# Kernel optimization log

Hardware: AMD Instinct MI355X
Metric: run time of the kernel (lower is better)

Reference implementation:

```python
import jax, jax.numpy as jnp
import numpy as np

R = 16
ALPHA = 32.0
SCALING = ALPHA / max(1, R)

def setup_inputs() -> dict:
    key = jax.random.key(0)
    ks = jax.random.split(key, 7)
    B_, D, M = 16384, 1024, 4096
    return {
        "x": jax.random.normal(ks[0], (B_, D), dtype=jnp.float32),
        "W0": jax.random.normal(ks[1], (M, D), dtype=jnp.float32) * 0.02,
        "b0": jax.random.normal(ks[2], (M,), dtype=jnp.float32) * 0.02,
        "A": jax.random.normal(ks[3], (R, D), dtype=jnp.float32) * 0.001,
        "B": jax.random.normal(ks[4], (M, R), dtype=jnp.float32) * 0.02,
        "W2": jax.random.normal(ks[5], (1, M), dtype=jnp.float32) * 0.02,
        "b2": jax.random.normal(ks[6], (1,), dtype=jnp.float32) * 0.02,
    }

def reference(x, W0, b0, A, B, W2, b2):
    # effective_W = W0 + scaling * (B @ A)  -> [m_hidden, d_in]
    W_eff = W0 + SCALING * (B @ A)
    # F.linear(x, W_eff, b0): x @ W_eff^T + b0 -> [batch, m_hidden]
    h = jax.nn.relu(jnp.einsum('bd,md->bm', x, W_eff) + b0)
    # fc2: [batch, 1] then squeeze(-1)
    out = (jnp.einsum('bm,om->bo', h, W2) + b2).squeeze(-1)
    return out
```

## Files before the change

### kernel.cpp

```cpp
#include <hip/hip_runtime.h>
#include <hip/hip_bf16.h>
#include <stdint.h>

#define BATCH  16384
#define D_IN   1024
#define M_HID  4096
#define R_LORA 16
#define SCALING 2.0f

#define BM 128
#define BN 128
#define BK 64

typedef __bf16 bf16x8 __attribute__((ext_vector_type(8)));
typedef float  f32x4  __attribute__((ext_vector_type(4)));


__device__ __forceinline__ unsigned short f2bf(float f) {
    union { float f; unsigned int u; } c; c.f = f;
    unsigned int u = c.u;
    return (unsigned short)((u + 0x7FFFu + ((u >> 16) & 1u)) >> 16);
}

#define PREP_X_BLOCKS   (BATCH * D_IN / 8 / 256)
#define PREP_W_BLOCKS   (M_HID * D_IN / 4 / 256)
#define PREP_O_BLOCKS   (BATCH / 256)
__global__ __launch_bounds__(256) void k_prep(
    const float* __restrict__ x, const float* __restrict__ W0,
    const float* __restrict__ A, const float* __restrict__ Bl,
    const float* __restrict__ b2,
    unsigned short* __restrict__ xb, unsigned short* __restrict__ wb,
    float* __restrict__ out)
{
    int bid = blockIdx.x;
    if (bid < PREP_X_BLOCKS) {
        int idx = bid * 256 + threadIdx.x;
        const float4* x4 = (const float4*)x;
        float4 a = x4[2 * idx], b = x4[2 * idx + 1];
        uint4 o;
        o.x = (unsigned)f2bf(a.x) | ((unsigned)f2bf(a.y) << 16);
        o.y = (unsigned)f2bf(a.z) | ((unsigned)f2bf(a.w) << 16);
        o.z = (unsigned)f2bf(b.x) | ((unsigned)f2bf(b.y) << 16);
        o.w = (unsigned)f2bf(b.z) | ((unsigned)f2bf(b.w) << 16);
        ((uint4*)xb)[idx] = o;
    } else if (bid < PREP_X_BLOCKS + PREP_W_BLOCKS) {
        int idx = (bid - PREP_X_BLOCKS) * 256 + threadIdx.x;
        int m  = idx >> 8;
        int d4 = idx & 255;
        float4 acc = ((const float4*)W0)[idx];
        const float* brow = Bl + m * R_LORA;
#pragma unroll
        for (int r = 0; r < R_LORA; ++r) {
            float s = SCALING * brow[r];
            float4 a4 = ((const float4*)(A + r * D_IN))[d4];
            acc.x += s * a4.x; acc.y += s * a4.y; acc.z += s * a4.z; acc.w += s * a4.w;
        }
        uint2 o;
        o.x = (unsigned)f2bf(acc.x) | ((unsigned)f2bf(acc.y) << 16);
        o.y = (unsigned)f2bf(acc.z) | ((unsigned)f2bf(acc.w) << 16);
        ((uint2*)wb)[idx] = o;
    } else {
        int i = (bid - PREP_X_BLOCKS - PREP_W_BLOCKS) * 256 + threadIdx.x;
        out[i] = b2[0];
    }
}

template<bool XBF, bool WBF>
__global__ __launch_bounds__(256) void k_gemm_fused(
    const unsigned short* __restrict__ xb, const float* __restrict__ xf,
    const unsigned short* __restrict__ wb,
    const float* __restrict__ W0, const float* __restrict__ A,
    const float* __restrict__ Bl,
    const float* __restrict__ b0, const float* __restrict__ W2,
    float* __restrict__ out)
{
    __shared__ unsigned short As[BM * BK];
    __shared__ unsigned short Bs[BN * BK];

    const int tid  = threadIdx.x;
    const int lane = tid & 63;
    const int wave = tid >> 6;
    const int col0 = blockIdx.x * BN;
    const int row0 = blockIdx.y * BM;
    const int wm = (wave & 1) * 64;
    const int wn = (wave >> 1) * 64;
    const int cl = lane & 15, q = lane >> 4;

    f32x4 acc[4][4] = {};

    for (int k0 = 0; k0 < D_IN; k0 += BK) {
        if (XBF) {
#pragma unroll
            for (int it = 0; it < 4; ++it) {
                int c = it * 256 + tid;
                int r = c >> 3, s = c & 7;
                int k = s ^ (r & 7);
                const unsigned short* g = xb + (row0 + r) * D_IN + k0 + k * 8;
                __builtin_amdgcn_global_load_lds(
                    (__attribute__((address_space(1))) void*)g,
                    (__attribute__((address_space(3))) void*)(&As[c * 8]),
                    16, 0, 0);
            }
        } else {
#pragma unroll
            for (int it = 0; it < 8; ++it) {
                int gidx = it * 256 + tid;
                int r = gidx >> 4, kc = (gidx & 15) * 4;
                float4 v = *(const float4*)(xf + (size_t)(row0 + r) * D_IN + k0 + kc);
                ushort4 o = make_ushort4(f2bf(v.x), f2bf(v.y), f2bf(v.z), f2bf(v.w));
                int k = kc >> 3, half = (gidx & 1) * 4;
                *(ushort4*)(&As[r * BK + (k ^ (r & 7)) * 8 + half]) = o;
            }
        }
        if (WBF) {
#pragma unroll
            for (int it = 0; it < 4; ++it) {
                int c = it * 256 + tid;
                int r = c >> 3, s = c & 7;
                int k = s ^ (r & 7);
                const unsigned short* g = wb + (col0 + r) * D_IN + k0 + k * 8;
                __builtin_amdgcn_global_load_lds(
                    (__attribute__((address_space(1))) void*)g,
                    (__attribute__((address_space(3))) void*)(&Bs[c * 8]),
                    16, 0, 0);
            }
        } else {
#pragma unroll
            for (int it = 0; it < 8; ++it) {
                int gidx = it * 256 + tid;
                int n = gidx >> 4, kc = (gidx & 15) * 4;
                float4 v = *(const float4*)(W0 + (size_t)(col0 + n) * D_IN + k0 + kc);
                const float* brow = Bl + (col0 + n) * R_LORA;
#pragma unroll
                for (int r = 0; r < R_LORA; ++r) {
                    float s = SCALING * brow[r];
                    float4 a4 = *(const float4*)(A + r * D_IN + k0 + kc);
                    v.x += s * a4.x; v.y += s * a4.y; v.z += s * a4.z; v.w += s * a4.w;
                }
                ushort4 o = make_ushort4(f2bf(v.x), f2bf(v.y), f2bf(v.z), f2bf(v.w));
                int k = kc >> 3, half = (gidx & 1) * 4;
                *(ushort4*)(&Bs[n * BK + (k ^ (n & 7)) * 8 + half]) = o;
            }
        }
        __syncthreads();

#pragma unroll
        for (int kk = 0; kk < BK; kk += 32) {
            const int chunk = (kk >> 3) + q;
            const int sA = chunk ^ (cl & 7);
            bf16x8 af[4], bfr[4];
#pragma unroll
            for (int t = 0; t < 4; ++t)
                af[t] = *(const bf16x8*)(&As[(wm + t * 16 + cl) * BK + sA * 8]);
#pragma unroll
            for (int t = 0; t < 4; ++t)
                bfr[t] = *(const bf16x8*)(&Bs[(wn + t * 16 + cl) * BK + sA * 8]);
#pragma unroll
            for (int ti = 0; ti < 4; ++ti)
#pragma unroll
                for (int tj = 0; tj < 4; ++tj)
                    acc[ti][tj] = __builtin_amdgcn_mfma_f32_16x16x32_bf16(
                        af[ti], bfr[tj], acc[ti][tj], 0, 0, 0);
        }
        __syncthreads();
    }

    const int r_base = row0 + wm + q * 4;
    const int c_base = col0 + wn + cl;
#pragma unroll
    for (int ti = 0; ti < 4; ++ti) {
        float p0 = 0.f, p1 = 0.f, p2 = 0.f, p3 = 0.f;
#pragma unroll
        for (int tj = 0; tj < 4; ++tj) {
            int hid = c_base + tj * 16;
            float w2 = W2[hid], bb = b0[hid];
            f32x4 a = acc[ti][tj];
            p0 += fmaxf(a[0] + bb, 0.f) * w2;
            p1 += fmaxf(a[1] + bb, 0.f) * w2;
            p2 += fmaxf(a[2] + bb, 0.f) * w2;
            p3 += fmaxf(a[3] + bb, 0.f) * w2;
        }
#pragma unroll
        for (int m = 1; m <= 8; m <<= 1) {
            p0 += __shfl_xor(p0, m, 64);
            p1 += __shfl_xor(p1, m, 64);
            p2 += __shfl_xor(p2, m, 64);
            p3 += __shfl_xor(p3, m, 64);
        }
        if (cl == 0) {
            int rr = r_base + ti * 16;
            unsafeAtomicAdd(&out[rr + 0], p0);
            unsafeAtomicAdd(&out[rr + 1], p1);
            unsafeAtomicAdd(&out[rr + 2], p2);
            unsafeAtomicAdd(&out[rr + 3], p3);
        }
    }
}

extern "C" void kernel_launch(void* const* d_in, const int* in_sizes, int n_in,
                              void* d_out, int out_size, void* d_ws, size_t ws_size,
                              hipStream_t stream) {
    const float* x  = (const float*)d_in[0];
    const float* W0 = (const float*)d_in[1];
    const float* b0 = (const float*)d_in[2];
    const float* A  = (const float*)d_in[3];
    const float* Bl = (const float*)d_in[4];
    const float* W2 = (const float*)d_in[5];
    const float* b2 = (const float*)d_in[6];
    float* out = (float*)d_out;

    const size_t wb_bytes = (size_t)M_HID * D_IN * 2;
    const size_t xb_bytes = (size_t)BATCH * D_IN * 2;
    const bool have_ws = ws_size >= wb_bytes + xb_bytes;
    unsigned short* wb = (unsigned short*)d_ws;
    unsigned short* xb = (unsigned short*)((char*)d_ws + wb_bytes);

    dim3 grid(M_HID / BN, BATCH / BM);

    if (have_ws) {
        hipLaunchKernelGGL(k_prep, dim3(PREP_X_BLOCKS + PREP_W_BLOCKS + PREP_O_BLOCKS),
                           dim3(256), 0, stream, x, W0, A, Bl, b2, xb, wb, out);
        hipLaunchKernelGGL((k_gemm_fused<true, true>), grid, dim3(256), 0, stream,
                           xb, x, wb, W0, A, Bl, b0, W2, out);
    } else {
        hipLaunchKernelGGL(k_prep, dim3(PREP_O_BLOCKS), dim3(256), 0, stream,
                           x, W0, A, Bl, b2, xb, wb, out);
        hipLaunchKernelGGL((k_gemm_fused<false, false>), grid, dim3(256), 0, stream,
                           xb, x, wb, W0, A, Bl, b0, W2, out);
    }
}
```

Before: 309.5 us.

## Enlarge GEMM tile to 256x128 with 8 waves and 32x32x16 MFMA

Doubles the row tile to 256 and the block to 512 threads (8 waves), and switches the inner product from 16x16x32 to 32x32x16 bf16 MFMA with 2x2 fragments per wave. Each loaded W tile now serves twice as many rows, and the larger MFMA shape cuts LDS fragment reads per flop. The epilogue now reduces over 32 lanes and issues one atomic per row per wave. The cost is more LDS per block (48KB) and fewer resident blocks. The fallback path also gets a separate init kernel.

```diff
diff --git a/kernel.cpp b/kernel.cpp
--- a/kernel.cpp
+++ b/kernel.cpp
@@ -8,12 +8,13 @@
 #define R_LORA 16
 #define SCALING 2.0f
 
-#define BM 128
+#define BM 256
 #define BN 128
 #define BK 64
+#define NTHREADS 512
 
 typedef __bf16 bf16x8 __attribute__((ext_vector_type(8)));
-typedef float  f32x4  __attribute__((ext_vector_type(4)));
+typedef float  f32x16 __attribute__((ext_vector_type(16)));
 
 
 __device__ __forceinline__ unsigned short f2bf(float f) {
@@ -65,8 +66,13 @@
     }
 }
 
-template<bool XBF, bool WBF>
-__global__ __launch_bounds__(256) void k_gemm_fused(
+__global__ __launch_bounds__(256) void k_init_out(float* __restrict__ out,
+                                                  const float* __restrict__ b2) {
+    out[blockIdx.x * 256 + threadIdx.x] = b2[0];
+}
+
+template<bool FAST>
+__global__ __launch_bounds__(NTHREADS) void k_gemm_fused(
     const unsigned short* __restrict__ xb, const float* __restrict__ xf,
     const unsigned short* __restrict__ wb,
     const float* __restrict__ W0, const float* __restrict__ A,
@@ -82,17 +88,18 @@
     const int wave = tid >> 6;
     const int col0 = blockIdx.x * BN;
     const int row0 = blockIdx.y * BM;
-    const int wm = (wave & 1) * 64;
-    const int wn = (wave >> 1) * 64;
-    const int cl = lane & 15, q = lane >> 4;
-
-    f32x4 acc[4][4] = {};
+    const int wm = (wave & 3) * 64;
+    const int wn = (wave >> 2) * 64;
+    const int rl   = lane & 31;
+    const int half = lane >> 5;
+
+    f32x16 acc[2][2] = {};
 
     for (int k0 = 0; k0 < D_IN; k0 += BK) {
-        if (XBF) {
+        if (FAST) {
 #pragma unroll
             for (int it = 0; it < 4; ++it) {
-                int c = it * 256 + tid;
+                int c = it * NTHREADS + tid;
                 int r = c >> 3, s = c & 7;
                 int k = s ^ (r & 7);
                 const unsigned short* g = xb + (row0 + r) * D_IN + k0 + k * 8;
@@ -101,21 +108,9 @@
                     (__attribute__((address_space(3))) void*)(&As[c * 8]),
                     16, 0, 0);
             }
-        } else {
-#pragma unroll
-            for (int it = 0; it < 8; ++it) {
-                int gidx = it * 256 + tid;
-                int r = gidx >> 4, kc = (gidx & 15) * 4;
-                float4 v = *(const float4*)(xf + (size_t)(row0 + r) * D_IN + k0 + kc);
-                ushort4 o = make_ushort4(f2bf(v.x), f2bf(v.y), f2bf(v.z), f2bf(v.w));
-                int k = kc >> 3, half = (gidx & 1) * 4;
-                *(ushort4*)(&As[r * BK + (k ^ (r & 7)) * 8 + half]) = o;
-            }
-        }
-        if (WBF) {
-#pragma unroll
-            for (int it = 0; it < 4; ++it) {
-                int c = it * 256 + tid;
+#pragma unroll
+            for (int it = 0; it < 2; ++it) {
+                int c = it * NTHREADS + tid;
                 int r = c >> 3, s = c & 7;
                 int k = s ^ (r & 7);
                 const unsigned short* g = wb + (col0 + r) * D_IN + k0 + k * 8;
@@ -127,7 +122,16 @@
         } else {
 #pragma unroll
             for (int it = 0; it < 8; ++it) {
-                int gidx = it * 256 + tid;
+                int gidx = it * NTHREADS + tid;
+                int r = gidx >> 4, kc = (gidx & 15) * 4;
+                float4 v = *(const float4*)(xf + (size_t)(row0 + r) * D_IN + k0 + kc);
+                ushort4 o = make_ushort4(f2bf(v.x), f2bf(v.y), f2bf(v.z), f2bf(v.w));
+                int k = kc >> 3, h4 = (gidx & 1) * 4;
+                *(ushort4*)(&As[r * BK + ((k ^ (r & 7)) * 8) + h4]) = o;
+            }
+#pragma unroll
+            for (int it = 0; it < 4; ++it) {
+                int gidx = it * NTHREADS + tid;
                 int n = gidx >> 4, kc = (gidx & 15) * 4;
                 float4 v = *(const float4*)(W0 + (size_t)(col0 + n) * D_IN + k0 + kc);
                 const float* brow = Bl + (col0 + n) * R_LORA;
@@ -138,61 +142,49 @@
                     v.x += s * a4.x; v.y += s * a4.y; v.z += s * a4.z; v.w += s * a4.w;
                 }
                 ushort4 o = make_ushort4(f2bf(v.x), f2bf(v.y), f2bf(v.z), f2bf(v.w));
-                int k = kc >> 3, half = (gidx & 1) * 4;
-                *(ushort4*)(&Bs[n * BK + (k ^ (n & 7)) * 8 + half]) = o;
+                int k = kc >> 3, h4 = (gidx & 1) * 4;
+                *(ushort4*)(&Bs[n * BK + ((k ^ (n & 7)) * 8) + h4]) = o;
             }
         }
         __syncthreads();
 
 #pragma unroll
-        for (int kk = 0; kk < BK; kk += 32) {
-            const int chunk = (kk >> 3) + q;
-            const int sA = chunk ^ (cl & 7);
-            bf16x8 af[4], bfr[4];
-#pragma unroll
-            for (int t = 0; t < 4; ++t)
-                af[t] = *(const bf16x8*)(&As[(wm + t * 16 + cl) * BK + sA * 8]);
-#pragma unroll
-            for (int t = 0; t < 4; ++t)
-                bfr[t] = *(const bf16x8*)(&Bs[(wn + t * 16 + cl) * BK + sA * 8]);
-#pragma unroll
-            for (int ti = 0; ti < 4; ++ti)
-#pragma unroll
-                for (int tj = 0; tj < 4; ++tj)
-                    acc[ti][tj] = __builtin_amdgcn_mfma_f32_16x16x32_bf16(
+        for (int kk = 0; kk < BK; kk += 16) {
+            const int chunk = (kk >> 3) + half;
+            const int slot  = chunk ^ (rl & 7);
+            bf16x8 af[2], bfr[2];
+#pragma unroll
+            for (int t = 0; t < 2; ++t)
+                af[t] = *(const bf16x8*)(&As[(wm + t * 32 + rl) * BK + slot * 8]);
+#pragma unroll
+            for (int t = 0; t < 2; ++t)
+                bfr[t] = *(const bf16x8*)(&Bs[(wn + t * 32 + rl) * BK + slot * 8]);
+#pragma unroll
+            for (int ti = 0; ti < 2; ++ti)
+#pragma unroll
+                for (int tj = 0; tj < 2; ++tj)
+                    acc[ti][tj] = __builtin_amdgcn_mfma_f32_32x32x16_bf16(
                         af[ti], bfr[tj], acc[ti][tj], 0, 0, 0);
         }
         __syncthreads();
     }
 
-    const int r_base = row0 + wm + q * 4;
-    const int c_base = col0 + wn + cl;
-#pragma unroll
-    for (int ti = 0; ti < 4; ++ti) {
-        float p0 = 0.f, p1 = 0.f, p2 = 0.f, p3 = 0.f;
-#pragma unroll
-        for (int tj = 0; tj < 4; ++tj) {
-            int hid = c_base + tj * 16;
-            float w2 = W2[hid], bb = b0[hid];
-            f32x4 a = acc[ti][tj];
-            p0 += fmaxf(a[0] + bb, 0.f) * w2;
-            p1 += fmaxf(a[1] + bb, 0.f) * w2;
-            p2 += fmaxf(a[2] + bb, 0.f) * w2;
-            p3 += fmaxf(a[3] + bb, 0.f) * w2;
-        }
-#pragma unroll
-        for (int m = 1; m <= 8; m <<= 1) {
-            p0 += __shfl_xor(p0, m, 64);
-            p1 += __shfl_xor(p1, m, 64);
-            p2 += __shfl_xor(p2, m, 64);
-            p3 += __shfl_xor(p3, m, 64);
-        }
-        if (cl == 0) {
-            int rr = r_base + ti * 16;
-            unsafeAtomicAdd(&out[rr + 0], p0);
-            unsafeAtomicAdd(&out[rr + 1], p1);
-            unsafeAtomicAdd(&out[rr + 2], p2);
-            unsafeAtomicAdd(&out[rr + 3], p3);
+    const int hid0 = col0 + wn + rl;
+    const float w2a = W2[hid0],      bba = b0[hid0];
+    const float w2b = W2[hid0 + 32], bbb = b0[hid0 + 32];
+#pragma unroll
+    for (int ti = 0; ti < 2; ++ti) {
+#pragma unroll
+        for (int r = 0; r < 16; ++r) {
+            float p = fmaxf(acc[ti][0][r] + bba, 0.f) * w2a
+                    + fmaxf(acc[ti][1][r] + bbb, 0.f) * w2b;
+#pragma unroll
+            for (int m = 1; m <= 16; m <<= 1)
+                p += __shfl_xor(p, m, 64);
+            if (rl == 0) {
+                int row = row0 + wm + ti * 32 + (r & 3) + 8 * (r >> 2) + 4 * half;
+                unsafeAtomicAdd(&out[row], p);
+            }
         }
     }
 }
@@ -220,12 +212,11 @@
     if (have_ws) {
         hipLaunchKernelGGL(k_prep, dim3(PREP_X_BLOCKS + PREP_W_BLOCKS + PREP_O_BLOCKS),
                            dim3(256), 0, stream, x, W0, A, Bl, b2, xb, wb, out);
-        hipLaunchKernelGGL((k_gemm_fused<true, true>), grid, dim3(256), 0, stream,
+        hipLaunchKernelGGL((k_gemm_fused<true>), grid, dim3(NTHREADS), 0, stream,
                            xb, x, wb, W0, A, Bl, b0, W2, out);
     } else {
-        hipLaunchKernelGGL(k_prep, dim3(PREP_O_BLOCKS), dim3(256), 0, stream,
-                           x, W0, A, Bl, b2, xb, wb, out);
-        hipLaunchKernelGGL((k_gemm_fused<false, false>), grid, dim3(256), 0, stream,
+        hipLaunchKernelGGL(k_init_out, dim3(PREP_O_BLOCKS), dim3(256), 0, stream, out, b2);
+        hipLaunchKernelGGL((k_gemm_fused<false>), grid, dim3(NTHREADS), 0, stream,
                            xb, x, wb, W0, A, Bl, b0, W2, out);
     }
 }
```

Result: no change. 312.0 us (+0.8%).
